# Optimization experiments

Measured on AMD Instinct MI355X. Metric: run time of the kernel, lower is better.

The kernel has to match this reference:

```python
import jax, jax.numpy as jnp
import numpy as np

TEMPERATURE = 1.0
WEIGHT = 1.0


def _transitivity_sum(rel):
    """rel: [N, N] relation probabilities for one (batch, relation) slice.
    Computes sum_{a,b,c} relu(rel[a,b] - rel[a,c] * rel[b,c]) via a scan over c
    (outer product of column c), keeping memory at O(N^2) instead of O(N^3)."""
    def step(acc, col):  # col = rel[:, c], shape [N]
        viol = jax.nn.relu(rel - col[:, None] * col[None, :])  # [N, N]
        return acc + jnp.sum(viol), None
    acc, _ = jax.lax.scan(step, jnp.zeros((), rel.dtype), rel.T)
    return acc


def setup_inputs() -> dict:
    key = jax.random.key(0)
    B, N, R = 2, 512, 4
    relation_logits = jax.random.normal(key, (B, N, N, R), dtype=jnp.float32)
    entity_masks = jnp.ones((B, N), dtype=jnp.int32)
    return {"relation_logits": relation_logits, "entity_masks": entity_masks}


def reference(relation_logits, entity_masks):
    B, N, _, R = relation_logits.shape
    probs = jax.nn.sigmoid(relation_logits / TEMPERATURE)  # [B, N, N, R]
    m = (entity_masks > 0).astype(probs.dtype)             # [B, N]
    rel = probs * m[:, :, None, None] * m[:, None, :, None]
    # flatten (batch, relation) and vmap the per-matrix cubic reduction
    rel_br = jnp.transpose(rel, (0, 3, 1, 2)).reshape(B * R, N, N)
    per = jax.vmap(_transitivity_sum)(rel_br)              # [B*R]
    # per-batch loss = sum_r / R; final = weight * mean over batch
    return WEIGHT * jnp.sum(per) / (R * B)
```

## Files before the change

kernel.cpp:

```cpp
#include <hip/hip_runtime.h>
#include <math.h>

#define N      512
#define RNUM   4
#define BNUM   2
#define NSLICE (RNUM * BNUM)
#define TILE   128
#define CT     32
#define LSTR   136
#define CSPLIT 16
#define NCOLB  16
#define SCALE  0.0625f

typedef _Float16 half2_t __attribute__((ext_vector_type(2)));

__device__ __forceinline__ unsigned int h2u(half2_t h) {
  return __builtin_bit_cast(unsigned int, h);
}
__device__ __forceinline__ half2_t u2h(unsigned int u) {
  return __builtin_bit_cast(half2_t, u);
}

#if __has_builtin(__builtin_amdgcn_fdot2)
__device__ __forceinline__ float fdot2_(half2_t a, half2_t b, float c) {
  return __builtin_amdgcn_fdot2(a, b, c, false);
}
#else
__device__ __forceinline__ float fdot2_(half2_t a, half2_t b, float c) {
  return c + (float)a.x * (float)b.x + (float)a.y * (float)b.y;
}
#endif

__device__ __forceinline__ float sigmoidf_(float x) {
  return 1.0f / (1.0f + __expf(-x));
}

__global__ void zero_out_kernel(float* out) { out[0] = 0.0f; }

__global__ __launch_bounds__(256) void prep_f16_kernel(const float* __restrict__ logits,
                                                       const int* __restrict__ masks,
                                                       _Float16* __restrict__ P,
                                                       float* __restrict__ out) {
  if (blockIdx.x == 0 && threadIdx.x == 0) out[0] = 0.0f;
  int t = blockIdx.x * 256 + threadIdx.x;
  int b = t >> 18;
  int rem = t & (N * N - 1);
  int i = rem >> 9;
  int j = rem & (N - 1);
  float4 lg = *(const float4*)(logits + (size_t)t * 4);
  float mm = ((masks[b * N + i] > 0) && (masks[b * N + j] > 0)) ? 1.0f : 0.0f;
  size_t base = (size_t)b * RNUM * N * N + rem;
  P[base + 0 * (size_t)N * N] = (_Float16)(mm * sigmoidf_(lg.x));
  P[base + 1 * (size_t)N * N] = (_Float16)(mm * sigmoidf_(lg.y));
  P[base + 2 * (size_t)N * N] = (_Float16)(mm * sigmoidf_(lg.z));
  P[base + 3 * (size_t)N * N] = (_Float16)(mm * sigmoidf_(lg.w));
}

__global__ __launch_bounds__(256) void work_f16_kernel(const _Float16* __restrict__ P,
                                                       float* __restrict__ out) {
  __shared__ _Float16 tA[CT][LSTR];
  __shared__ _Float16 tB[CT][LSTR];
  __shared__ float wsum[4];

  const int tid = threadIdx.x;
  const int bid = blockIdx.x;

  if (bid < NCOLB) {
    const int s    = bid >> 1;
    const int half = bid & 1;
    const int c    = half * 256 + tid;
    const _Float16* col = P + (size_t)s * N * N + c;
    float sum = 0.0f;
#pragma unroll 8
    for (int a = 0; a < N; ++a) sum += (float)col[(size_t)a * N];
    float v = sum * ((float)N - sum);
    for (int off = 32; off > 0; off >>= 1) v += __shfl_down(v, off, 64);
    const int wid = tid >> 6;
    if ((tid & 63) == 0) wsum[wid] = v;
    __syncthreads();
    if (tid == 0)
      atomicAdd(out, (wsum[0] + wsum[1] + wsum[2] + wsum[3]) * SCALE);
    return;
  }

  const int m  = bid - NCOLB;
  const int bt = m & 3;
  const int at = (m >> 2) & 3;
  const int s  = (m >> 4) & 7;
  const int cz = m >> 7;
  const int a0 = at * TILE;
  const int b0 = bt * TILE;
  const int c0 = cz * CT;

  const int ta = tid & 15;
  const int tb = tid >> 4;

  const _Float16* Ph = P + (size_t)s * N * N;

  half2_t rab2[8][4];
#pragma unroll
  for (int x = 0; x < 8; ++x) {
    int ga = a0 + ((x >> 2) << 6) + ta * 4 + (x & 3);
    uint2 u0 = *(const uint2*)(Ph + (size_t)ga * N + b0 + tb * 4);
    uint2 u1 = *(const uint2*)(Ph + (size_t)ga * N + b0 + 64 + tb * 4);
    rab2[x][0] = u2h(u0.x); rab2[x][1] = u2h(u0.y);
    rab2[x][2] = u2h(u1.x); rab2[x][3] = u2h(u1.y);
  }

  float acc[8];
#pragma unroll
  for (int x = 0; x < 8; ++x) acc[x] = 0.0f;

  const half2_t kOne = {(_Float16)1.0f, (_Float16)1.0f};

  {
    const int sx   = tid & 127;
    const int sarr = tid >> 7;
    const _Float16* srow = Ph + (size_t)((sarr ? b0 : a0) + sx) * N;
    _Float16* dcol = sarr ? &tB[0][sx] : &tA[0][sx];
    const uint4* src = (const uint4*)(srow + c0);
    uint4 q0 = src[0];
    uint4 q1 = src[1];
    uint4 q2 = src[2];
    uint4 q3 = src[3];
    unsigned int w[16] = {q0.x, q0.y, q0.z, q0.w, q1.x, q1.y, q1.z, q1.w,
                          q2.x, q2.y, q2.z, q2.w, q3.x, q3.y, q3.z, q3.w};
    union { unsigned int u32; _Float16 h[2]; } cv;
#pragma unroll
    for (int k = 0; k < 16; ++k) {
      cv.u32 = w[k];
      dcol[(size_t)(2 * k) * LSTR]     = cv.h[0];
      dcol[(size_t)(2 * k + 1) * LSTR] = cv.h[1];
    }
  }
  __syncthreads();

#pragma unroll 4
  for (int c = 0; c < CT; ++c) {
    uint2 ua0 = *(const uint2*)&tA[c][ta * 4];
    uint2 ua1 = *(const uint2*)&tA[c][64 + ta * 4];
    uint2 ub0 = *(const uint2*)&tB[c][tb * 4];
    uint2 ub1 = *(const uint2*)&tB[c][64 + tb * 4];
    half2_t av[4] = {u2h(ua0.x), u2h(ua0.y), u2h(ua1.x), u2h(ua1.y)};
    half2_t bv[4] = {u2h(ub0.x), u2h(ub0.y), u2h(ub1.x), u2h(ub1.y)};
#pragma unroll
    for (int x = 0; x < 8; ++x) {
      _Float16 as = (x & 1) ? av[x >> 1].y : av[x >> 1].x;
      half2_t asp = {as, as};
      float a_ = acc[x];
#pragma unroll
      for (int yp = 0; yp < 4; ++yp) {
        half2_t t2 = rab2[x][yp] - asp * bv[yp];
        half2_t p2 = u2h(h2u(t2) & 0x7FFF7FFFu);
        a_ = fdot2_(p2, kOne, a_);
      }
      acc[x] = a_;
    }
  }

  float tsum = 0.0f;
#pragma unroll
  for (int x = 0; x < 8; ++x) tsum += acc[x];

  for (int off = 32; off > 0; off >>= 1) tsum += __shfl_down(tsum, off, 64);

  const int wid = tid >> 6;
  if ((tid & 63) == 0) wsum[wid] = tsum;
  __syncthreads();
  if (tid == 0)
    atomicAdd(out, (wsum[0] + wsum[1] + wsum[2] + wsum[3]) * SCALE);
}

#define FCT    64
#define FSTR   132
#define FCSPL  4

__global__ __launch_bounds__(256, 2) void work_f32_fallback(const float* __restrict__ logits,
                                                            const int* __restrict__ masks,
                                                            float* __restrict__ out) {
  __shared__ __align__(16) float tA[FCT][FSTR];
  __shared__ __align__(16) float tB[FCT][FSTR];
  __shared__ float wsum[4];

  const int tid = threadIdx.x;
  const int bid = blockIdx.x;

  if (bid < NCOLB) {
    const int s    = bid >> 1;
    const int half = bid & 1;
    const int c    = half * 256 + tid;
    const int bb   = s >> 2;
    const int r    = s & 3;
    const int* mrow = masks + bb * N;
    float mc = (mrow[c] > 0) ? 1.0f : 0.0f;
    float sum = 0.0f;
#pragma unroll 4
    for (int a = 0; a < N; ++a) {
      float ma = (mrow[a] > 0) ? 1.0f : 0.0f;
      size_t idx = ((size_t)(bb * N + a) * N + c) * RNUM + r;
      sum += sigmoidf_(logits[idx]) * ma * mc;
    }
    float v = sum * ((float)N - sum);
    for (int off = 32; off > 0; off >>= 1) v += __shfl_down(v, off, 64);
    const int wid = tid >> 6;
    if ((tid & 63) == 0) wsum[wid] = v;
    __syncthreads();
    if (tid == 0)
      atomicAdd(out, (wsum[0] + wsum[1] + wsum[2] + wsum[3]) * SCALE);
    return;
  }

  const int m  = bid - NCOLB;
  const int bt = m & 3;
  const int at = (m >> 2) & 3;
  const int s  = (m >> 4) & 7;
  const int cz = m >> 7;
  const int a0 = at * TILE;
  const int b0 = bt * TILE;
  const int bb = s >> 2;
  const int r  = s & 3;
  const int cbeg = cz * (N / FCSPL);
  const int cend = cbeg + (N / FCSPL);

  const int ta = tid & 15;
  const int tb = tid >> 4;
  const int* mrow = masks + bb * N;

  float rab[8][8];
#pragma unroll
  for (int x = 0; x < 8; ++x) {
    int ra = a0 + ((x >> 2) << 6) + ta * 4 + (x & 3);
    float ma = (mrow[ra] > 0) ? 1.0f : 0.0f;
#pragma unroll
    for (int y = 0; y < 8; ++y) {
      int cb = b0 + ((y >> 2) << 6) + tb * 4 + (y & 3);
      float mb = (mrow[cb] > 0) ? 1.0f : 0.0f;
      size_t idx = ((size_t)(bb * N + ra) * N + cb) * RNUM + r;
      rab[x][y] = sigmoidf_(logits[idx]) * ma * mb;
    }
  }

  float acc[8][2];
#pragma unroll
  for (int x = 0; x < 8; ++x) { acc[x][0] = 0.0f; acc[x][1] = 0.0f; }

  for (int c0 = cbeg; c0 < cend; c0 += FCT) {
    __syncthreads();
#pragma unroll
    for (int it = 0; it < 32; ++it) {
      int e = it * 256 + tid;
      int c = e & 63;
      int i = e >> 6;
      int pc = ((((i >> 2) ^ ((c >> 2) & 31)) & 31) << 2) | (i & 3);
      float mc = (mrow[c0 + c] > 0) ? 1.0f : 0.0f;
      {
        float mi = (mrow[a0 + i] > 0) ? 1.0f : 0.0f;
        size_t idx = ((size_t)(bb * N + a0 + i) * N + (c0 + c)) * RNUM + r;
        tA[c][pc] = sigmoidf_(logits[idx]) * mi * mc;
      }
      {
        float mi = (mrow[b0 + i] > 0) ? 1.0f : 0.0f;
        size_t idx = ((size_t)(bb * N + b0 + i) * N + (c0 + c)) * RNUM + r;
        tB[c][pc] = sigmoidf_(logits[idx]) * mi * mc;
      }
    }
    __syncthreads();

#pragma unroll 2
    for (int cg = 0; cg < FCT / 4; ++cg) {
      const float* pa = &tA[cg * 4][((ta ^ cg) & 31) << 2];
      const float* pb = &tB[cg * 4][((tb ^ cg) & 31) << 2];
#pragma unroll
      for (int dc = 0; dc < 4; ++dc) {
        float4 a0v = *(const float4*)(pa + dc * FSTR);
        float4 a1v = *(const float4*)(pa + dc * FSTR + 64);
        float4 b0v = *(const float4*)(pb + dc * FSTR);
        float4 b1v = *(const float4*)(pb + dc * FSTR + 64);
        float avv[8] = {a0v.x, a0v.y, a0v.z, a0v.w, a1v.x, a1v.y, a1v.z, a1v.w};
        float bvv[8] = {b0v.x, b0v.y, b0v.z, b0v.w, b1v.x, b1v.y, b1v.z, b1v.w};
#pragma unroll
        for (int x = 0; x < 8; ++x) {
#pragma unroll
          for (int y = 0; y < 4; ++y)
            acc[x][0] += fabsf(fmaf(-avv[x], bvv[y], rab[x][y]));
#pragma unroll
          for (int y = 4; y < 8; ++y)
            acc[x][1] += fabsf(fmaf(-avv[x], bvv[y], rab[x][y]));
        }
      }
    }
  }

  float tsum = 0.0f;
#pragma unroll
  for (int x = 0; x < 8; ++x) tsum += acc[x][0] + acc[x][1];
  for (int off = 32; off > 0; off >>= 1) tsum += __shfl_down(tsum, off, 64);
  const int wid = tid >> 6;
  if ((tid & 63) == 0) wsum[wid] = tsum;
  __syncthreads();
  if (tid == 0)
    atomicAdd(out, (wsum[0] + wsum[1] + wsum[2] + wsum[3]) * SCALE);
}

extern "C" void kernel_launch(void* const* d_in, const int* in_sizes, int n_in,
                              void* d_out, int out_size, void* d_ws, size_t ws_size,
                              hipStream_t stream) {
  const float* logits = (const float*)d_in[0];
  const int*   masks  = (const int*)d_in[1];
  float*       out    = (float*)d_out;

  const size_t P_BYTES = (size_t)NSLICE * N * N * sizeof(_Float16);

  if (ws_size >= P_BYTES) {
    _Float16* P = (_Float16*)d_ws;
    prep_f16_kernel<<<(BNUM * N * N) / 256, 256, 0, stream>>>(logits, masks, P, out);
    const int nblocks = NCOLB + 4 * 4 * NSLICE * CSPLIT;
    work_f16_kernel<<<nblocks, 256, 0, stream>>>(P, out);
  } else {
    zero_out_kernel<<<1, 1, 0, stream>>>(out);
    const int nblocks = NCOLB + 4 * 4 * NSLICE * FCSPL;
    work_f32_fallback<<<nblocks, 256, 0, stream>>>(logits, masks, out);
  }
}
```

Baseline: 114.1 us.

## Double c-tile depth, halve block count, and pack transposed LDS staging stores

Raises the per-block c-chunk from 32 to 64 and halves the c-split, so each block reuses its register-resident rab tile across twice as many columns and fewer blocks reload it. The LDS transpose staging now has each thread load two adjacent rows and write packed 32-bit half pairs, halving LDS store instructions, and it is moved ahead of the rab register loads so the global loads can overlap. It also adds a launch-bounds occupancy hint and unrolls the column-sum loop further. The cost is doubled LDS per block and fewer blocks available for parallelism.

New measurement: 117.3 us. +2.8%, slower.

```diff
diff --git a/kernel.cpp b/kernel.cpp
--- a/kernel.cpp
+++ b/kernel.cpp
@@ -6,9 +6,9 @@
 #define BNUM   2
 #define NSLICE (RNUM * BNUM)
 #define TILE   128
-#define CT     32
+#define CT     64
 #define LSTR   136
-#define CSPLIT 16
+#define CSPLIT 8
 #define NCOLB  16
 #define SCALE  0.0625f
 
@@ -56,8 +56,8 @@
   P[base + 3 * (size_t)N * N] = (_Float16)(mm * sigmoidf_(lg.w));
 }
 
-__global__ __launch_bounds__(256) void work_f16_kernel(const _Float16* __restrict__ P,
-                                                       float* __restrict__ out) {
+__global__ __launch_bounds__(256, 4) void work_f16_kernel(const _Float16* __restrict__ P,
+                                                          float* __restrict__ out) {
   __shared__ _Float16 tA[CT][LSTR];
   __shared__ _Float16 tB[CT][LSTR];
   __shared__ float wsum[4];
@@ -71,7 +71,7 @@
     const int c    = half * 256 + tid;
     const _Float16* col = P + (size_t)s * N * N + c;
     float sum = 0.0f;
-#pragma unroll 8
+#pragma unroll 16
     for (int a = 0; a < N; ++a) sum += (float)col[(size_t)a * N];
     float v = sum * ((float)N - sum);
     for (int off = 32; off > 0; off >>= 1) v += __shfl_down(v, off, 64);
@@ -97,6 +97,37 @@
 
   const _Float16* Ph = P + (size_t)s * N * N;
 
+  {
+    const int u   = tid & 127;
+    const int h   = tid >> 7;
+    const int isB = u >> 6;
+    const int p   = u & 63;
+    const int r0  = (isB ? b0 : a0) + 2 * p;
+    const int cc0 = c0 + h * 32;
+    const _Float16* s0row = Ph + (size_t)r0 * N + cc0;
+    const _Float16* s1row = s0row + N;
+    _Float16* dst = isB ? &tB[h * 32][2 * p] : &tA[h * 32][2 * p];
+    uint4 q0 = ((const uint4*)s0row)[0];
+    uint4 q1 = ((const uint4*)s0row)[1];
+    uint4 q2 = ((const uint4*)s0row)[2];
+    uint4 q3 = ((const uint4*)s0row)[3];
+    uint4 p0 = ((const uint4*)s1row)[0];
+    uint4 p1 = ((const uint4*)s1row)[1];
+    uint4 p2 = ((const uint4*)s1row)[2];
+    uint4 p3 = ((const uint4*)s1row)[3];
+    unsigned int w0[16] = {q0.x, q0.y, q0.z, q0.w, q1.x, q1.y, q1.z, q1.w,
+                           q2.x, q2.y, q2.z, q2.w, q3.x, q3.y, q3.z, q3.w};
+    unsigned int w1[16] = {p0.x, p0.y, p0.z, p0.w, p1.x, p1.y, p1.z, p1.w,
+                           p2.x, p2.y, p2.z, p2.w, p3.x, p3.y, p3.z, p3.w};
+#pragma unroll
+    for (int k = 0; k < 16; ++k) {
+      unsigned int lo = (w1[k] << 16) | (w0[k] & 0xFFFFu);
+      unsigned int hi = (w1[k] & 0xFFFF0000u) | (w0[k] >> 16);
+      *(unsigned int*)(dst + (size_t)(2 * k) * LSTR)     = lo;
+      *(unsigned int*)(dst + (size_t)(2 * k + 1) * LSTR) = hi;
+    }
+  }
+
   half2_t rab2[8][4];
 #pragma unroll
   for (int x = 0; x < 8; ++x) {
@@ -113,26 +144,6 @@
 
   const half2_t kOne = {(_Float16)1.0f, (_Float16)1.0f};
 
-  {
-    const int sx   = tid & 127;
-    const int sarr = tid >> 7;
-    const _Float16* srow = Ph + (size_t)((sarr ? b0 : a0) + sx) * N;
-    _Float16* dcol = sarr ? &tB[0][sx] : &tA[0][sx];
-    const uint4* src = (const uint4*)(srow + c0);
-    uint4 q0 = src[0];
-    uint4 q1 = src[1];
-    uint4 q2 = src[2];
-    uint4 q3 = src[3];
-    unsigned int w[16] = {q0.x, q0.y, q0.z, q0.w, q1.x, q1.y, q1.z, q1.w,
-                          q2.x, q2.y, q2.z, q2.w, q3.x, q3.y, q3.z, q3.w};
-    union { unsigned int u32; _Float16 h[2]; } cv;
-#pragma unroll
-    for (int k = 0; k < 16; ++k) {
-      cv.u32 = w[k];
-      dcol[(size_t)(2 * k) * LSTR]     = cv.h[0];
-      dcol[(size_t)(2 * k + 1) * LSTR] = cv.h[1];
-    }
-  }
   __syncthreads();
 
 #pragma unroll 4
```
